# Kernel optimization log

Hardware: AMD Instinct MI355X
Metric: run time of the kernel (lower is better)

Reference implementation:

```python
import jax, jax.numpy as jnp
import numpy as np

TEMPERATURE = 0.1
EPS = 1e-8  # torch cosine_similarity eps
NEG_FILL = -9e15

def setup_inputs() -> dict:
    key = jax.random.key(0)
    stacked_batch = jax.random.normal(key, (8192, 128), dtype=jnp.float32)
    return {"stacked_batch": stacked_batch}

def reference(stacked_batch) -> jnp.ndarray:
    n = stacked_batch.shape[0]
    # cosine similarity = normalized GEMM (equivalent to torch broadcast form)
    norm = jnp.maximum(jnp.linalg.norm(stacked_batch, axis=-1, keepdims=True), EPS)
    z = stacked_batch / norm                      # [N, D]
    sim = jnp.matmul(z, z.T) / TEMPERATURE        # [N, N]
    # mask self-similarity on the diagonal
    idx = jnp.arange(n)
    sim = sim.at[idx, idx].set(NEG_FILL)
    # positive pair for row i is column (i + N/2) mod N
    pos_cols = (idx + n // 2) % n
    pos = sim[idx, pos_cols]                      # [N]
    loss = jax.scipy.special.logsumexp(sim, axis=-1) - pos
    return loss.mean()
```

## Files before the change

### kernel.cpp

```cpp
#include <hip/hip_runtime.h>
#include <hip/hip_bf16.h>

#define N 8192
#define D 128
#define HALF_N 4096
#define SQRT_SCALE_LOG2E 3.79828236f
#define LN2 0.693147180559945f

#define BLOCK_ROWS 256
#define COLS_PER_ITER 64
#define COL_SPLITS 16
#define COLS_PER_BLOCK (N / COL_SPLITS)
#define ITERS (COLS_PER_BLOCK / COLS_PER_ITER)
#define LDS_STRIDE 136

typedef short frag8 __attribute__((ext_vector_type(8)));
typedef float f32x4 __attribute__((ext_vector_type(4)));

#define OFF_POS    0
#define OFF_PSUMS  (N)
#define OFF_ACC    (N + COL_SPLITS * N)
#define OFF_Z_BYTES ((OFF_ACC + 64) * 4)

__device__ __forceinline__ unsigned short f2bf(float f) {
    unsigned int u = __float_as_uint(f);
    u += 0x7FFFu + ((u >> 16) & 1u);
    return (unsigned short)(u >> 16);
}

__global__ __launch_bounds__(256) void k_normalize(const float* __restrict__ x,
                                                   unsigned short* __restrict__ z,
                                                   float* __restrict__ acc0) {
    const int row  = blockIdx.x * 4 + (threadIdx.x >> 6);
    const int lane = threadIdx.x & 63;
    float2 v = ((const float2*)x)[row * 64 + lane];
    float s = v.x * v.x + v.y * v.y;
    #pragma unroll
    for (int m = 32; m >= 1; m >>= 1) s += __shfl_xor(s, m);
    float inv = SQRT_SCALE_LOG2E / fmaxf(sqrtf(s), 1e-8f);
    ushort2 o;
    o.x = f2bf(v.x * inv);
    o.y = f2bf(v.y * inv);
    ((ushort2*)z)[row * 64 + lane] = o;
    if (blockIdx.x == 0 && threadIdx.x == 0) acc0[0] = 0.0f;
}

__global__ __launch_bounds__(256, 2) void k_simloss(const unsigned short* __restrict__ z,
                                                    float* __restrict__ psums,
                                                    float* __restrict__ pos) {
    __shared__ unsigned short lds[COLS_PER_ITER * LDS_STRIDE];

    const int tid  = threadIdx.x;
    const int wave = tid >> 6;
    const int lane = tid & 63;
    const int l15  = lane & 15;
    const int quad = lane >> 4;
    const int wrow = blockIdx.x * BLOCK_ROWS + wave * 64;
    const int colbase0 = blockIdx.y * COLS_PER_BLOCK;
    const int posbase  = (wrow + HALF_N) & (N - 1);

    frag8 a[4][4];
    #pragma unroll
    for (int s = 0; s < 4; ++s) {
        const uint4* p = (const uint4*)&z[(wrow + s * 16 + l15) * D + quad * 8];
        #pragma unroll
        for (int q = 0; q < 4; ++q) {
            uint4 t = p[q * 4];
            a[s][q] = *(frag8*)&t;
        }
    }

    float sums[4][4];
    #pragma unroll
    for (int s = 0; s < 4; ++s)
        #pragma unroll
        for (int r = 0; r < 4; ++r) sums[s][r] = 0.0f;

    for (int it = 0; it < ITERS; ++it) {
        const int colbase = colbase0 + it * COLS_PER_ITER;
        __syncthreads();
        #pragma unroll
        for (int u = 0; u < 4; ++u) {
            int idx = u * 256 + tid;
            int r   = idx >> 4;
            int c8  = idx & 15;
            uint4 t = *(const uint4*)&z[(colbase + r) * D + c8 * 8];
            *(uint4*)&lds[r * LDS_STRIDE + c8 * 8] = t;
        }
        __syncthreads();

        const bool isDiag = (colbase == wrow);
        const bool isPos  = (colbase == posbase);
        const unsigned short* lp = &lds[l15 * LDS_STRIDE + quad * 8];

        #pragma unroll
        for (int c = 0; c < 4; ++c) {
            f32x4 acc[4];
            #pragma unroll
            for (int s = 0; s < 4; ++s) acc[s] = (f32x4){0.f, 0.f, 0.f, 0.f};
            #pragma unroll
            for (int q = 0; q < 4; ++q) {
                frag8 b = *(const frag8*)(lp + c * 16 * LDS_STRIDE + q * 32);
                #pragma unroll
                for (int s = 0; s < 4; ++s)
                    acc[s] = __builtin_amdgcn_mfma_f32_16x16x32_bf16(a[s][q], b, acc[s], 0, 0, 0);
            }
            if (isDiag | isPos) {
                #pragma unroll
                for (int s = 0; s < 4; ++s)
                    #pragma unroll
                    for (int r = 0; r < 4; ++r) {
                        float v = acc[s][r];
                        float e = __builtin_amdgcn_exp2f(v);
                        if (c == s) {
                            bool hit = (l15 == quad * 4 + r);
                            if (isDiag && hit) e = 0.0f;
                            if (isPos  && hit) pos[wrow + s * 16 + quad * 4 + r] = v * LN2;
                        }
                        sums[s][r] += e;
                    }
            } else {
                #pragma unroll
                for (int s = 0; s < 4; ++s)
                    #pragma unroll
                    for (int r = 0; r < 4; ++r)
                        sums[s][r] += __builtin_amdgcn_exp2f(acc[s][r]);
            }
        }
    }

    #pragma unroll
    for (int s = 0; s < 4; ++s)
        #pragma unroll
        for (int r = 0; r < 4; ++r) {
            float v = sums[s][r];
            v += __shfl_xor(v, 1);
            v += __shfl_xor(v, 2);
            v += __shfl_xor(v, 4);
            v += __shfl_xor(v, 8);
            if (l15 == 0)
                psums[blockIdx.y * N + wrow + s * 16 + quad * 4 + r] = v;
        }
}

__global__ __launch_bounds__(1024) void k_rowloss(const float* __restrict__ psums,
                                                  const float* __restrict__ pos,
                                                  float* __restrict__ acc0) {
    const int row = blockIdx.x * 1024 + threadIdx.x;
    float t = 0.0f;
    #pragma unroll
    for (int s = 0; s < COL_SPLITS; ++s) t += psums[s * N + row];
    float loss = __logf(t) - pos[row];
    #pragma unroll
    for (int m = 32; m >= 1; m >>= 1) loss += __shfl_xor(loss, m);
    __shared__ float p[16];
    if ((threadIdx.x & 63) == 0) p[threadIdx.x >> 6] = loss;
    __syncthreads();
    if (threadIdx.x == 0) {
        float s = 0.0f;
        #pragma unroll
        for (int w = 0; w < 16; ++w) s += p[w];
        atomicAdd(acc0, s);
    }
}

__global__ void k_final(const float* __restrict__ acc0, float* __restrict__ out) {
    out[0] = acc0[0] * (1.0f / N);
}

extern "C" void kernel_launch(void* const* d_in, const int* in_sizes, int n_in,
                              void* d_out, int out_size, void* d_ws, size_t ws_size,
                              hipStream_t stream) {
    const float* x = (const float*)d_in[0];
    float* wsf   = (float*)d_ws;
    float* pos   = wsf + OFF_POS;
    float* psums = wsf + OFF_PSUMS;
    float* acc0  = wsf + OFF_ACC;
    unsigned short* z = (unsigned short*)((char*)d_ws + OFF_Z_BYTES);

    k_normalize<<<N / 4, 256, 0, stream>>>(x, z, acc0);
    dim3 g2(N / BLOCK_ROWS, COL_SPLITS);
    k_simloss<<<g2, 256, 0, stream>>>(z, psums, pos);
    k_rowloss<<<N / 1024, 1024, 0, stream>>>(psums, pos, acc0);
    k_final<<<1, 1, 0, stream>>>(acc0, (float*)d_out);
}
```

Baseline: 83.93 us.

## Double-buffer column tiles via async global_load_lds with XOR-swizzled LDS layout

Column tiles are now staged into a double-buffered LDS array with direct global-to-LDS loads, so the next tile's load overlaps the MFMA and exp work on the current one. The padded layout is replaced by an XOR swizzle to avoid bank conflicts without padding. COL_SPLITS is doubled and the launch bound raised to 4 blocks per CU for more parallelism. The cost is more partial sums for the row-reduction kernel to combine and tighter register limits, which could cause spills given the 64 A-fragment registers per thread.

```diff
diff --git a/kernel.cpp b/kernel.cpp
--- a/kernel.cpp
+++ b/kernel.cpp
@@ -9,13 +9,14 @@
 
 #define BLOCK_ROWS 256
 #define COLS_PER_ITER 64
-#define COL_SPLITS 16
+#define COL_SPLITS 32
 #define COLS_PER_BLOCK (N / COL_SPLITS)
 #define ITERS (COLS_PER_BLOCK / COLS_PER_ITER)
-#define LDS_STRIDE 136
 
 typedef short frag8 __attribute__((ext_vector_type(8)));
 typedef float f32x4 __attribute__((ext_vector_type(4)));
+typedef const __attribute__((address_space(1))) unsigned int* gbl_u32p;
+typedef __attribute__((address_space(3))) unsigned int* lds_u32p;
 
 #define OFF_POS    0
 #define OFF_PSUMS  (N)
@@ -45,19 +46,45 @@
     if (blockIdx.x == 0 && threadIdx.x == 0) acc0[0] = 0.0f;
 }
 
-__global__ __launch_bounds__(256, 2) void k_simloss(const unsigned short* __restrict__ z,
+__device__ __forceinline__ void stage_tile(const unsigned short* __restrict__ z,
+                                           unsigned short* ldsbuf,
+                                           int colbase, int wave,
+                                           const int* stg_src) {
+    const unsigned short* zc = z + (size_t)colbase * D;
+    #pragma unroll
+    for (int u = 0; u < 4; ++u) {
+        __builtin_amdgcn_global_load_lds((gbl_u32p)(zc + stg_src[u]),
+                                         (lds_u32p)(ldsbuf + (wave * 16 + u * 4) * D),
+                                         16, 0, 0);
+    }
+}
+
+__global__ __launch_bounds__(256, 4) void k_simloss(const unsigned short* __restrict__ z,
                                                     float* __restrict__ psums,
                                                     float* __restrict__ pos) {
-    __shared__ unsigned short lds[COLS_PER_ITER * LDS_STRIDE];
+    __shared__ unsigned short lds[2][COLS_PER_ITER * D];
 
     const int tid  = threadIdx.x;
     const int wave = tid >> 6;
     const int lane = tid & 63;
     const int l15  = lane & 15;
     const int quad = lane >> 4;
+    const int l7   = l15 & 7;
     const int wrow = blockIdx.x * BLOCK_ROWS + wave * 64;
     const int colbase0 = blockIdx.y * COLS_PER_BLOCK;
     const int posbase  = (wrow + HALF_N) & (N - 1);
+
+    int stg_src[4];
+    #pragma unroll
+    for (int u = 0; u < 4; ++u) {
+        int r = wave * 16 + u * 4 + (lane >> 4);
+        stg_src[u] = r * D + ((l15 ^ (r & 7)) << 3);
+    }
+
+    int boff[4];
+    #pragma unroll
+    for (int q = 0; q < 4; ++q)
+        boff[q] = l15 * D + (((quad + 4 * q) ^ l7) << 3);
 
     frag8 a[4][4];
     #pragma unroll
@@ -76,22 +103,17 @@
         #pragma unroll
         for (int r = 0; r < 4; ++r) sums[s][r] = 0.0f;
 
+    stage_tile(z, &lds[0][0], colbase0, wave, stg_src);
+    __syncthreads();
+
     for (int it = 0; it < ITERS; ++it) {
+        if (it + 1 < ITERS)
+            stage_tile(z, &lds[(it + 1) & 1][0], colbase0 + (it + 1) * COLS_PER_ITER, wave, stg_src);
+
         const int colbase = colbase0 + it * COLS_PER_ITER;
-        __syncthreads();
-        #pragma unroll
-        for (int u = 0; u < 4; ++u) {
-            int idx = u * 256 + tid;
-            int r   = idx >> 4;
-            int c8  = idx & 15;
-            uint4 t = *(const uint4*)&z[(colbase + r) * D + c8 * 8];
-            *(uint4*)&lds[r * LDS_STRIDE + c8 * 8] = t;
-        }
-        __syncthreads();
-
         const bool isDiag = (colbase == wrow);
         const bool isPos  = (colbase == posbase);
-        const unsigned short* lp = &lds[l15 * LDS_STRIDE + quad * 8];
+        const unsigned short* lb = &lds[it & 1][0];
 
         #pragma unroll
         for (int c = 0; c < 4; ++c) {
@@ -100,7 +122,7 @@
             for (int s = 0; s < 4; ++s) acc[s] = (f32x4){0.f, 0.f, 0.f, 0.f};
             #pragma unroll
             for (int q = 0; q < 4; ++q) {
-                frag8 b = *(const frag8*)(lp + c * 16 * LDS_STRIDE + q * 32);
+                frag8 b = *(const frag8*)&lb[c * (16 * D) + boff[q]];
                 #pragma unroll
                 for (int s = 0; s < 4; ++s)
                     acc[s] = __builtin_amdgcn_mfma_f32_16x16x32_bf16(a[s][q], b, acc[s], 0, 0, 0);
@@ -127,6 +149,7 @@
                         sums[s][r] += __builtin_amdgcn_exp2f(acc[s][r]);
             }
         }
+        __syncthreads();
     }
 
     #pragma unroll
```

Measured after the change: 157.9 us. +88.2%, slower.

## Load B fragments directly from global with register double buffering, drop LDS staging

Applied to the files above, without the earlier changes.

Removes the shared-memory staging of column tiles and the two block-wide barriers per iteration. Each wave now reads its B fragments straight from global memory (expected to hit L1/L2) in 16-column subtiles. It double-buffers them in registers so the next subtile's loads overlap the current MFMAs and exp work. The trade-off is that the four waves of a block each fetch the same column data, which multiplies cache traffic. The final prefetch also reads one subtile past the block's column range, which for the last column split falls outside z.

```diff
diff --git a/kernel.cpp b/kernel.cpp
--- a/kernel.cpp
+++ b/kernel.cpp
@@ -8,11 +8,9 @@
 #define LN2 0.693147180559945f
 
 #define BLOCK_ROWS 256
-#define COLS_PER_ITER 64
 #define COL_SPLITS 16
 #define COLS_PER_BLOCK (N / COL_SPLITS)
-#define ITERS (COLS_PER_BLOCK / COLS_PER_ITER)
-#define LDS_STRIDE 136
+#define SUBTILES (COLS_PER_BLOCK / 16)
 
 typedef short frag8 __attribute__((ext_vector_type(8)));
 typedef float f32x4 __attribute__((ext_vector_type(4)));
@@ -48,8 +46,6 @@
 __global__ __launch_bounds__(256, 2) void k_simloss(const unsigned short* __restrict__ z,
                                                     float* __restrict__ psums,
                                                     float* __restrict__ pos) {
-    __shared__ unsigned short lds[COLS_PER_ITER * LDS_STRIDE];
-
     const int tid  = threadIdx.x;
     const int wave = tid >> 6;
     const int lane = tid & 63;
@@ -76,57 +72,62 @@
         #pragma unroll
         for (int r = 0; r < 4; ++r) sums[s][r] = 0.0f;
 
-    for (int it = 0; it < ITERS; ++it) {
-        const int colbase = colbase0 + it * COLS_PER_ITER;
-        __syncthreads();
+    const unsigned short* zlane = z + l15 * D + quad * 8;
+
+    auto load_b = [&](frag8 (&b)[4], int t) {
+        const unsigned short* bp = zlane + (colbase0 + t * 16) * D;
         #pragma unroll
-        for (int u = 0; u < 4; ++u) {
-            int idx = u * 256 + tid;
-            int r   = idx >> 4;
-            int c8  = idx & 15;
-            uint4 t = *(const uint4*)&z[(colbase + r) * D + c8 * 8];
-            *(uint4*)&lds[r * LDS_STRIDE + c8 * 8] = t;
+        for (int q = 0; q < 4; ++q)
+            b[q] = *(const frag8*)(bp + q * 32);
+    };
+
+    auto compute_tile = [&](int t, frag8 (&b)[4]) {
+        f32x4 acc[4];
+        #pragma unroll
+        for (int s = 0; s < 4; ++s) acc[s] = (f32x4){0.f, 0.f, 0.f, 0.f};
+        #pragma unroll
+        for (int q = 0; q < 4; ++q)
+            #pragma unroll
+            for (int s = 0; s < 4; ++s)
+                acc[s] = __builtin_amdgcn_mfma_f32_16x16x32_bf16(a[s][q], b[q], acc[s], 0, 0, 0);
+
+        const int col0 = colbase0 + t * 16;
+        const unsigned dd = (unsigned)(col0 - wrow);
+        const unsigned pp = (unsigned)(col0 - posbase);
+        if ((dd < 64u) | (pp < 64u)) {
+            #pragma unroll
+            for (int s = 0; s < 4; ++s) {
+                const bool d = (col0 == wrow + s * 16);
+                const bool p = (col0 == posbase + s * 16);
+                #pragma unroll
+                for (int r = 0; r < 4; ++r) {
+                    float v = acc[s][r];
+                    float e = __builtin_amdgcn_exp2f(v);
+                    if (d | p) {
+                        bool hit = (l15 == quad * 4 + r);
+                        if (d && hit) e = 0.0f;
+                        if (p && hit) pos[wrow + s * 16 + quad * 4 + r] = v * LN2;
+                    }
+                    sums[s][r] += e;
+                }
+            }
+        } else {
+            #pragma unroll
+            for (int s = 0; s < 4; ++s)
+                #pragma unroll
+                for (int r = 0; r < 4; ++r)
+                    sums[s][r] += __builtin_amdgcn_exp2f(acc[s][r]);
         }
-        __syncthreads();
+    };
 
-        const bool isDiag = (colbase == wrow);
-        const bool isPos  = (colbase == posbase);
-        const unsigned short* lp = &lds[l15 * LDS_STRIDE + quad * 8];
-
-        #pragma unroll
-        for (int c = 0; c < 4; ++c) {
-            f32x4 acc[4];
-            #pragma unroll
-            for (int s = 0; s < 4; ++s) acc[s] = (f32x4){0.f, 0.f, 0.f, 0.f};
-            #pragma unroll
-            for (int q = 0; q < 4; ++q) {
-                frag8 b = *(const frag8*)(lp + c * 16 * LDS_STRIDE + q * 32);
-                #pragma unroll
-                for (int s = 0; s < 4; ++s)
-                    acc[s] = __builtin_amdgcn_mfma_f32_16x16x32_bf16(a[s][q], b, acc[s], 0, 0, 0);
-            }
-            if (isDiag | isPos) {
-                #pragma unroll
-                for (int s = 0; s < 4; ++s)
-                    #pragma unroll
-                    for (int r = 0; r < 4; ++r) {
-                        float v = acc[s][r];
-                        float e = __builtin_amdgcn_exp2f(v);
-                        if (c == s) {
-                            bool hit = (l15 == quad * 4 + r);
-                            if (isDiag && hit) e = 0.0f;
-                            if (isPos  && hit) pos[wrow + s * 16 + quad * 4 + r] = v * LN2;
-                        }
-                        sums[s][r] += e;
-                    }
-            } else {
-                #pragma unroll
-                for (int s = 0; s < 4; ++s)
-                    #pragma unroll
-                    for (int r = 0; r < 4; ++r)
-                        sums[s][r] += __builtin_amdgcn_exp2f(acc[s][r]);
-            }
-        }
+    frag8 b0[4], b1[4];
+    load_b(b0, 0);
+    #pragma unroll 1
+    for (int t = 0; t < SUBTILES; t += 2) {
+        load_b(b1, t + 1);
+        compute_tile(t, b0);
+        load_b(b0, t + 2);
+        compute_tile(t + 1, b1);
     }
 
     #pragma unroll
```

New measurement: 96.72 us. 1.15x slower.
